# Kernel optimization log

Measured on AMD Instinct MI355X. Metric: run time of the kernel, lower is better.

Reference implementation:

```python
import jax, jax.numpy as jnp
import numpy as np

D_EMBED = 768
D_HEAD = 64
B, S = 4, 4096


def setup_inputs() -> dict:
    key = jax.random.key(0)
    ks = jax.random.split(key, 8)
    x = jax.random.normal(ks[0], (B, S, D_EMBED), dtype=jnp.float32)
    mask = jax.random.randint(ks[1], (B, S), 0, 2, dtype=jnp.int32)
    s = 1.0 / np.sqrt(D_EMBED)
    Wq = jax.random.normal(ks[2], (D_EMBED, D_HEAD), dtype=jnp.float32) * s
    bq = jnp.zeros((D_HEAD,), dtype=jnp.float32)
    Wk = jax.random.normal(ks[3], (D_EMBED, D_HEAD), dtype=jnp.float32) * s
    bk = jnp.zeros((D_HEAD,), dtype=jnp.float32)
    Wv = jax.random.normal(ks[4], (D_EMBED, D_HEAD), dtype=jnp.float32) * s
    bv = jnp.zeros((D_HEAD,), dtype=jnp.float32)
    return {"x": x, "mask": mask, "Wq": Wq, "bq": bq, "Wk": Wk, "bk": bk, "Wv": Wv, "bv": bv}


def reference(x, mask, Wq, bq, Wk, bk, Wv, bv):
    # x: [B,S,D_EMBED], mask: [B,S] (0 = masked)
    q = x @ Wq + bq          # [B,S,Dh]
    k = x @ Wk + bk
    v = x @ Wv + bv
    scale = jnp.float32(1.0 / np.sqrt(D_HEAD))
    scores = jnp.einsum('bsd,btd->bst', q, k) * scale   # [B,S,S]
    scores = jnp.where(mask[:, None, :] == 0, jnp.float32(-1e9), scores)
    probs = jax.nn.softmax(scores, axis=-1)
    return jnp.einsum('bst,btd->bsd', probs, v)          # [B,S,Dh]
```

## Files before the change

### kernel.cpp

```cpp
#include <hip/hip_runtime.h>
#include <hip/hip_bf16.h>
#include <stdint.h>

#define B_  4
#define S_  4096
#define DE  768
#define DH  64
#define NQKV 192
#define MFIX 8.0f
#define NSPLIT 8
#define QG 128

typedef __attribute__((ext_vector_type(8))) short    short8;
typedef __attribute__((ext_vector_type(4))) float    floatx4;
typedef __attribute__((ext_vector_type(4))) unsigned short ushort4v;

__device__ unsigned short g_wt[NQKV * DE];
__device__ unsigned short g_q [B_ * S_ * DH];
__device__ unsigned short g_k [B_ * S_ * DH];
__device__ unsigned short g_vt[B_ * DH * S_];
__device__ float g_po[(size_t)B_ * 32 * NSPLIT * QG * DH];
__device__ float g_pl[(size_t)B_ * 32 * NSPLIT * QG];

__device__ __forceinline__ unsigned short f2bf_h(float f) {
    union { float f; uint32_t u; } v; v.f = f;
    return (unsigned short)((v.u + 0x8000u) >> 16);
}

__global__ __launch_bounds__(256) void pack_w(
    const float* __restrict__ Wq, const float* __restrict__ Wk,
    const float* __restrict__ Wv)
{
    int idx = blockIdx.x * 256 + threadIdx.x;
    if (idx >= NQKV * DE) return;
    int n = idx / DE;
    int d = idx - n * DE;
    float w;
    if      (n < 64)  w = Wq[d * 64 + n];
    else if (n < 128) w = Wk[d * 64 + (n - 64)];
    else              w = Wv[d * 64 + (n - 128)];
    g_wt[idx] = f2bf_h(w);
}

__global__ __launch_bounds__(256, 3) void qkv_mfma(
    const float* __restrict__ x,
    const float* __restrict__ bq, const float* __restrict__ bk,
    const float* __restrict__ bv)
{
    __shared__ unsigned short xs[32][776];
    const int t    = threadIdx.x;
    const int lane = t & 63;
    const int wave = t >> 6;
    const int c16  = lane & 15;
    const int quad = lane >> 4;
    const int n0   = wave * 48;
    const int row0 = blockIdx.x * 32;

    {
        const int xr = t >> 3;
        const int xc = t & 7;
        const float* xrow = x + (size_t)(row0 + xr) * DE;
        #pragma unroll
        for (int j = 0; j < 24; ++j) {
            int c4 = xc + 8 * j;
            floatx4 v = *(const floatx4*)&xrow[c4 * 4];
            ushort4v h;
            #pragma unroll
            for (int k = 0; k < 4; ++k) h[k] = f2bf_h(v[k]);
            *(ushort4v*)&xs[xr][c4 * 4] = h;
        }
    }
    __syncthreads();

    floatx4 acc[6];
    #pragma unroll
    for (int i = 0; i < 6; ++i) acc[i] = (floatx4){0.f,0.f,0.f,0.f};

    short8 wb[6];
    #pragma unroll
    for (int nt = 0; nt < 3; ++nt) {
        const unsigned short* wrow = g_wt + (size_t)(n0 + nt * 16 + c16) * DE + quad * 8;
        wb[2 * nt]     = *(const short8*)wrow;
        wb[2 * nt + 1] = *(const short8*)(wrow + 32);
    }

    #pragma unroll
    for (int ks = 0; ks < 12; ++ks) {
        const int k0  = ks * 64;
        const int k0n = (ks < 11) ? k0 + 64 : 0;
        short8 nwb[6];
        #pragma unroll
        for (int nt = 0; nt < 3; ++nt) {
            const unsigned short* wrow = g_wt + (size_t)(n0 + nt * 16 + c16) * DE + k0n + quad * 8;
            nwb[2 * nt]     = *(const short8*)wrow;
            nwb[2 * nt + 1] = *(const short8*)(wrow + 32);
        }
        short8 a00 = *(const short8*)&xs[c16][k0 + quad * 8];
        short8 a01 = *(const short8*)&xs[c16][k0 + quad * 8 + 32];
        short8 a10 = *(const short8*)&xs[16 + c16][k0 + quad * 8];
        short8 a11 = *(const short8*)&xs[16 + c16][k0 + quad * 8 + 32];
        #pragma unroll
        for (int nt = 0; nt < 3; ++nt) {
            acc[nt]     = __builtin_amdgcn_mfma_f32_16x16x32_bf16(a00, wb[2 * nt],     acc[nt],     0, 0, 0);
            acc[nt]     = __builtin_amdgcn_mfma_f32_16x16x32_bf16(a01, wb[2 * nt + 1], acc[nt],     0, 0, 0);
            acc[3 + nt] = __builtin_amdgcn_mfma_f32_16x16x32_bf16(a10, wb[2 * nt],     acc[3 + nt], 0, 0, 0);
            acc[3 + nt] = __builtin_amdgcn_mfma_f32_16x16x32_bf16(a11, wb[2 * nt + 1], acc[3 + nt], 0, 0, 0);
        }
        #pragma unroll
        for (int j = 0; j < 6; ++j) wb[j] = nwb[j];
    }

    #pragma unroll
    for (int m = 0; m < 2; ++m) {
        const int tokb = row0 + m * 16 + quad * 4;
        #pragma unroll
        for (int nt = 0; nt < 3; ++nt) {
            int n = n0 + nt * 16 + c16;
            int which = n >> 6;
            int d = n & 63;
            float bias = (which == 0) ? bq[d] : (which == 1) ? bk[d] : bv[d];
            floatx4 a = acc[m * 3 + nt];
            if (which == 0) {
                #pragma unroll
                for (int r = 0; r < 4; ++r)
                    g_q[(size_t)(tokb + r) * DH + d] = f2bf_h((a[r] + bias) * 0.125f);
            } else if (which == 1) {
                #pragma unroll
                for (int r = 0; r < 4; ++r)
                    g_k[(size_t)(tokb + r) * DH + d] = f2bf_h(a[r] + bias);
            } else {
                ushort4v h;
                #pragma unroll
                for (int r = 0; r < 4; ++r) h[r] = f2bf_h(a[r] + bias);
                int b = tokb >> 12;
                int tloc = tokb & (S_ - 1);
                *(ushort4v*)&g_vt[((size_t)b * DH + d) * S_ + tloc] = h;
            }
        }
    }
}

__global__ __launch_bounds__(256, 4) void attn_kernel(const int* __restrict__ mask)
{
    __shared__ short8 ksv[512];
    __shared__ short8 vsv[512];
    __shared__ unsigned short sp[4 * 2 * 16 * 72];

    const int t    = threadIdx.x;
    const int lane = t & 63;
    const int wave = t >> 6;
    const int c16  = lane & 15;
    const int quad = lane >> 4;
    const int qg   = blockIdx.x;
    const int b    = blockIdx.y;
    const int s    = blockIdx.z;
    const size_t tok0 = (size_t)b * S_;
    const int pidx = (b * 32 + qg) * NSPLIT + s;

    const unsigned short* kbase = g_k + tok0 * DH;
    const unsigned short* vtb   = g_vt + (size_t)b * DH * S_;
    const int* mrow = mask + b * S_;

    short8 aq0A, aq1A, aq0B, aq1B;
    {
        const unsigned short* qrA = g_q + (tok0 + qg * QG + wave * 32 + c16) * DH;
        aq0A = *(const short8*)(qrA + quad * 8);
        aq1A = *(const short8*)(qrA + quad * 8 + 32);
        const unsigned short* qrB = qrA + 16 * DH;
        aq0B = *(const short8*)(qrB + quad * 8);
        aq1B = *(const short8*)(qrB + quad * 8 + 32);
    }

    short8 ones;
    #pragma unroll
    for (int j = 0; j < 8; ++j) ones[j] = (short)0x3F80;

    floatx4 acc[2][5];
    #pragma unroll
    for (int qt = 0; qt < 2; ++qt)
        #pragma unroll
        for (int i = 0; i < 5; ++i) acc[qt][i] = (floatx4){0.f,0.f,0.f,0.f};

    const int kbeg = s * (S_ / NSPLIT);
    const int kend = kbeg + S_ / NSPLIT;

    #define SPI(w, qt, row, col) ((((w) * 2 + (qt)) * 16 + (row)) * 72 + (col))

    const int sr  = t >> 2;
    const int sp0 = (t & 3) * 2;
    const int sw0 = sr * 8 + (sp0 ^ (sr & 7));
    const int sw1 = sr * 8 + ((sp0 + 1) ^ (sr & 7));

    short8 kpre0, kpre1, vpre0, vpre1;
    int mpre[4];
    {
        const unsigned short* kr = kbase + (size_t)(kbeg + sr) * DH + sp0 * 8;
        kpre0 = *(const short8*)kr;
        kpre1 = *(const short8*)(kr + 8);
        const unsigned short* vr = vtb + (size_t)sr * S_ + kbeg + sp0 * 8;
        vpre0 = *(const short8*)vr;
        vpre1 = *(const short8*)(vr + 8);
        #pragma unroll
        for (int nt = 0; nt < 4; ++nt) mpre[nt] = mrow[kbeg + c16 + 16 * nt];
    }

    for (int tb = kbeg; tb < kend; tb += 64) {
        __syncthreads();
        ksv[sw0] = kpre0;
        ksv[sw1] = kpre1;
        vsv[sw0] = vpre0;
        vsv[sw1] = vpre1;
        int mv[4];
        #pragma unroll
        for (int nt = 0; nt < 4; ++nt) mv[nt] = mpre[nt];
        __syncthreads();

        {
            const int tbn = (tb + 64 < kend) ? tb + 64 : kbeg;
            const unsigned short* kr = kbase + (size_t)(tbn + sr) * DH + sp0 * 8;
            kpre0 = *(const short8*)kr;
            kpre1 = *(const short8*)(kr + 8);
            const unsigned short* vr = vtb + (size_t)sr * S_ + tbn + sp0 * 8;
            vpre0 = *(const short8*)vr;
            vpre1 = *(const short8*)(vr + 8);
            #pragma unroll
            for (int nt = 0; nt < 4; ++nt) mpre[nt] = mrow[tbn + c16 + 16 * nt];
        }

        #pragma unroll
        for (int nt = 0; nt < 4; ++nt) {
            const int key = c16 + 16 * nt;
            short8 kb0 = ksv[key * 8 + (quad ^ (key & 7))];
            short8 kb1 = ksv[key * 8 + ((quad + 4) ^ (key & 7))];
            floatx4 zA = (floatx4){0.f,0.f,0.f,0.f};
            zA = __builtin_amdgcn_mfma_f32_16x16x32_bf16(aq0A, kb0, zA, 0, 0, 0);
            zA = __builtin_amdgcn_mfma_f32_16x16x32_bf16(aq1A, kb1, zA, 0, 0, 0);
            floatx4 zB = (floatx4){0.f,0.f,0.f,0.f};
            zB = __builtin_amdgcn_mfma_f32_16x16x32_bf16(aq0B, kb0, zB, 0, 0, 0);
            zB = __builtin_amdgcn_mfma_f32_16x16x32_bf16(aq1B, kb1, zB, 0, 0, 0);
            #pragma unroll
            for (int r = 0; r < 4; ++r) {
                float sA = mv[nt] ? zA[r] : -1e9f;
                float sB = mv[nt] ? zB[r] : -1e9f;
                sp[SPI(wave, 0, quad * 4 + r, key)] = f2bf_h(__expf(sA - MFIX));
                sp[SPI(wave, 1, quad * 4 + r, key)] = f2bf_h(__expf(sB - MFIX));
            }
        }

        #pragma unroll
        for (int h = 0; h < 2; ++h) {
            short8 apA = *(const short8*)&sp[SPI(wave, 0, c16, quad * 8 + 32 * h)];
            short8 apB = *(const short8*)&sp[SPI(wave, 1, c16, quad * 8 + 32 * h)];
            #pragma unroll
            for (int nt = 0; nt < 4; ++nt) {
                const int d = c16 + 16 * nt;
                short8 vb = vsv[d * 8 + ((h * 4 + quad) ^ (d & 7))];
                acc[0][nt] = __builtin_amdgcn_mfma_f32_16x16x32_bf16(apA, vb, acc[0][nt], 0, 0, 0);
                acc[1][nt] = __builtin_amdgcn_mfma_f32_16x16x32_bf16(apB, vb, acc[1][nt], 0, 0, 0);
            }
            acc[0][4] = __builtin_amdgcn_mfma_f32_16x16x32_bf16(apA, ones, acc[0][4], 0, 0, 0);
            acc[1][4] = __builtin_amdgcn_mfma_f32_16x16x32_bf16(apB, ones, acc[1][4], 0, 0, 0);
        }
    }

    float* po = g_po + (size_t)pidx * (QG * DH) + (wave * 32) * 64;
    #pragma unroll
    for (int qt = 0; qt < 2; ++qt)
        #pragma unroll
        for (int nt = 0; nt < 4; ++nt)
            #pragma unroll
            for (int r = 0; r < 4; ++r)
                po[(qt * 16 + quad * 4 + r) * 64 + c16 + 16 * nt] = acc[qt][nt][r];
    if (c16 == 0) {
        float* pl = g_pl + (size_t)pidx * QG + wave * 32;
        #pragma unroll
        for (int qt = 0; qt < 2; ++qt)
            #pragma unroll
            for (int r = 0; r < 4; ++r)
                pl[qt * 16 + quad * 4 + r] = acc[qt][4][r];
    }
}

__global__ __launch_bounds__(256) void combine(float* __restrict__ out)
{
    const int idx = blockIdx.x * 256 + threadIdx.x;
    const int d4  = idx & 15;
    const int tok = idx >> 4;
    const int qq  = tok & (QG - 1);
    const int qg  = (tok >> 7) & 31;
    const int b   = tok >> 12;
    const int base = (b * 32 + qg) * NSPLIT;
    floatx4 os = (floatx4){0.f,0.f,0.f,0.f};
    float ls = 0.f;
    #pragma unroll
    for (int s = 0; s < NSPLIT; ++s) {
        os += *(const floatx4*)&g_po[(size_t)(base + s) * (QG * DH) + qq * 64 + d4 * 4];
        ls += g_pl[(size_t)(base + s) * QG + qq];
    }
    float inv = 1.0f / ls;
    floatx4 r;
    #pragma unroll
    for (int j = 0; j < 4; ++j) r[j] = os[j] * inv;
    *(floatx4*)&out[(size_t)tok * DH + d4 * 4] = r;
}

extern "C" void kernel_launch(void* const* d_in, const int* in_sizes, int n_in,
                              void* d_out, int out_size, void* d_ws, size_t ws_size,
                              hipStream_t stream) {
    const float* x   = (const float*)d_in[0];
    const int*   msk = (const int*)  d_in[1];
    const float* Wq  = (const float*)d_in[2];
    const float* bq  = (const float*)d_in[3];
    const float* Wk  = (const float*)d_in[4];
    const float* bk  = (const float*)d_in[5];
    const float* Wv  = (const float*)d_in[6];
    const float* bv  = (const float*)d_in[7];
    float* out = (float*)d_out;

    pack_w<<<dim3((NQKV * DE + 255) / 256), 256, 0, stream>>>(Wq, Wk, Wv);
    qkv_mfma<<<dim3(B_ * S_ / 32), 256, 0, stream>>>(x, bq, bk, bv);
    attn_kernel<<<dim3(S_ / QG, B_, NSPLIT), 256, 0, stream>>>(msk);
    combine<<<dim3(B_ * S_ * DH / 1024), 256, 0, stream>>>(out);
}
```

Measured before the change: 151.2 us.

## Double query tile per block and store split partials in fp16

Each attention block now handles 256 queries (64 per wave, four 16-row MFMA tiles) instead of 128. Every K/V tile staged in shared memory is reused across twice as many queries, halving K/V global traffic and staging work. Partial outputs are written as fp16 rather than fp32, halving the scratch traffic between the attention and combine kernels. In exchange, register and LDS use per block grow (launch bounds drop to 2 blocks per CU), the grid has half as many blocks, and the fp16 partials lose some precision and could overflow for large unnormalized sums.

```diff
diff --git a/kernel.cpp b/kernel.cpp
--- a/kernel.cpp
+++ b/kernel.cpp
@@ -1,5 +1,6 @@
 #include <hip/hip_runtime.h>
 #include <hip/hip_bf16.h>
+#include <hip/hip_fp16.h>
 #include <stdint.h>
 
 #define B_  4
@@ -9,7 +10,7 @@
 #define NQKV 192
 #define MFIX 8.0f
 #define NSPLIT 8
-#define QG 128
+#define QG 256
 
 typedef __attribute__((ext_vector_type(8))) short    short8;
 typedef __attribute__((ext_vector_type(4))) float    floatx4;
@@ -19,8 +20,8 @@
 __device__ unsigned short g_q [B_ * S_ * DH];
 __device__ unsigned short g_k [B_ * S_ * DH];
 __device__ unsigned short g_vt[B_ * DH * S_];
-__device__ float g_po[(size_t)B_ * 32 * NSPLIT * QG * DH];
-__device__ float g_pl[(size_t)B_ * 32 * NSPLIT * QG];
+__device__ __half g_po[(size_t)B_ * (S_ / QG) * NSPLIT * QG * DH];
+__device__ float  g_pl[(size_t)B_ * (S_ / QG) * NSPLIT * QG];
 
 __device__ __forceinline__ unsigned short f2bf_h(float f) {
     union { float f; uint32_t u; } v; v.f = f;
@@ -140,11 +141,11 @@
     }
 }
 
-__global__ __launch_bounds__(256, 4) void attn_kernel(const int* __restrict__ mask)
+__global__ __launch_bounds__(256, 2) void attn_kernel(const int* __restrict__ mask)
 {
     __shared__ short8 ksv[512];
     __shared__ short8 vsv[512];
-    __shared__ unsigned short sp[4 * 2 * 16 * 72];
+    __shared__ unsigned short sp[4 * 4 * 16 * 72];
 
     const int t    = threadIdx.x;
     const int lane = t & 63;
@@ -155,36 +156,34 @@
     const int b    = blockIdx.y;
     const int s    = blockIdx.z;
     const size_t tok0 = (size_t)b * S_;
-    const int pidx = (b * 32 + qg) * NSPLIT + s;
+    const int pidx = (b * (S_ / QG) + qg) * NSPLIT + s;
 
     const unsigned short* kbase = g_k + tok0 * DH;
     const unsigned short* vtb   = g_vt + (size_t)b * DH * S_;
     const int* mrow = mask + b * S_;
 
-    short8 aq0A, aq1A, aq0B, aq1B;
-    {
-        const unsigned short* qrA = g_q + (tok0 + qg * QG + wave * 32 + c16) * DH;
-        aq0A = *(const short8*)(qrA + quad * 8);
-        aq1A = *(const short8*)(qrA + quad * 8 + 32);
-        const unsigned short* qrB = qrA + 16 * DH;
-        aq0B = *(const short8*)(qrB + quad * 8);
-        aq1B = *(const short8*)(qrB + quad * 8 + 32);
+    short8 aq[4][2];
+    #pragma unroll
+    for (int qt = 0; qt < 4; ++qt) {
+        const unsigned short* qr = g_q + (tok0 + qg * QG + wave * 64 + qt * 16 + c16) * DH;
+        aq[qt][0] = *(const short8*)(qr + quad * 8);
+        aq[qt][1] = *(const short8*)(qr + quad * 8 + 32);
     }
 
     short8 ones;
     #pragma unroll
     for (int j = 0; j < 8; ++j) ones[j] = (short)0x3F80;
 
-    floatx4 acc[2][5];
-    #pragma unroll
-    for (int qt = 0; qt < 2; ++qt)
+    floatx4 acc[4][5];
+    #pragma unroll
+    for (int qt = 0; qt < 4; ++qt)
         #pragma unroll
         for (int i = 0; i < 5; ++i) acc[qt][i] = (floatx4){0.f,0.f,0.f,0.f};
 
     const int kbeg = s * (S_ / NSPLIT);
     const int kend = kbeg + S_ / NSPLIT;
 
-    #define SPI(w, qt, row, col) ((((w) * 2 + (qt)) * 16 + (row)) * 72 + (col))
+    #define SPI(w, qt, row, col) ((((w) * 4 + (qt)) * 16 + (row)) * 72 + (col))
 
     const int sr  = t >> 2;
     const int sp0 = (t & 3) * 2;
@@ -232,52 +231,56 @@
             const int key = c16 + 16 * nt;
             short8 kb0 = ksv[key * 8 + (quad ^ (key & 7))];
             short8 kb1 = ksv[key * 8 + ((quad + 4) ^ (key & 7))];
-            floatx4 zA = (floatx4){0.f,0.f,0.f,0.f};
-            zA = __builtin_amdgcn_mfma_f32_16x16x32_bf16(aq0A, kb0, zA, 0, 0, 0);
-            zA = __builtin_amdgcn_mfma_f32_16x16x32_bf16(aq1A, kb1, zA, 0, 0, 0);
-            floatx4 zB = (floatx4){0.f,0.f,0.f,0.f};
-            zB = __builtin_amdgcn_mfma_f32_16x16x32_bf16(aq0B, kb0, zB, 0, 0, 0);
-            zB = __builtin_amdgcn_mfma_f32_16x16x32_bf16(aq1B, kb1, zB, 0, 0, 0);
-            #pragma unroll
-            for (int r = 0; r < 4; ++r) {
-                float sA = mv[nt] ? zA[r] : -1e9f;
-                float sB = mv[nt] ? zB[r] : -1e9f;
-                sp[SPI(wave, 0, quad * 4 + r, key)] = f2bf_h(__expf(sA - MFIX));
-                sp[SPI(wave, 1, quad * 4 + r, key)] = f2bf_h(__expf(sB - MFIX));
+            #pragma unroll
+            for (int qt = 0; qt < 4; ++qt) {
+                floatx4 z = (floatx4){0.f,0.f,0.f,0.f};
+                z = __builtin_amdgcn_mfma_f32_16x16x32_bf16(aq[qt][0], kb0, z, 0, 0, 0);
+                z = __builtin_amdgcn_mfma_f32_16x16x32_bf16(aq[qt][1], kb1, z, 0, 0, 0);
+                #pragma unroll
+                for (int r = 0; r < 4; ++r) {
+                    float sv = mv[nt] ? z[r] : -1e9f;
+                    sp[SPI(wave, qt, quad * 4 + r, key)] = f2bf_h(__expf(sv - MFIX));
+                }
             }
         }
 
         #pragma unroll
         for (int h = 0; h < 2; ++h) {
-            short8 apA = *(const short8*)&sp[SPI(wave, 0, c16, quad * 8 + 32 * h)];
-            short8 apB = *(const short8*)&sp[SPI(wave, 1, c16, quad * 8 + 32 * h)];
+            short8 ap[4];
+            #pragma unroll
+            for (int qt = 0; qt < 4; ++qt)
+                ap[qt] = *(const short8*)&sp[SPI(wave, qt, c16, quad * 8 + 32 * h)];
             #pragma unroll
             for (int nt = 0; nt < 4; ++nt) {
                 const int d = c16 + 16 * nt;
                 short8 vb = vsv[d * 8 + ((h * 4 + quad) ^ (d & 7))];
-                acc[0][nt] = __builtin_amdgcn_mfma_f32_16x16x32_bf16(apA, vb, acc[0][nt], 0, 0, 0);
-                acc[1][nt] = __builtin_amdgcn_mfma_f32_16x16x32_bf16(apB, vb, acc[1][nt], 0, 0, 0);
+                #pragma unroll
+                for (int qt = 0; qt < 4; ++qt)
+                    acc[qt][nt] = __builtin_amdgcn_mfma_f32_16x16x32_bf16(ap[qt], vb, acc[qt][nt], 0, 0, 0);
             }
-            acc[0][4] = __builtin_amdgcn_mfma_f32_16x16x32_bf16(apA, ones, acc[0][4], 0, 0, 0);
-            acc[1][4] = __builtin_amdgcn_mfma_f32_16x16x32_bf16(apB, ones, acc[1][4], 0, 0, 0);
-        }
-    }
-
-    float* po = g_po + (size_t)pidx * (QG * DH) + (wave * 32) * 64;
-    #pragma unroll
-    for (int qt = 0; qt < 2; ++qt)
+            #pragma unroll
+            for (int qt = 0; qt < 4; ++qt)
+                acc[qt][4] = __builtin_amdgcn_mfma_f32_16x16x32_bf16(ap[qt], ones, acc[qt][4], 0, 0, 0);
+        }
+    }
+
+    __half* po = g_po + (size_t)pidx * (QG * DH);
+    #pragma unroll
+    for (int qt = 0; qt < 4; ++qt) {
+        const int qrow = wave * 64 + qt * 16 + quad * 4;
         #pragma unroll
         for (int nt = 0; nt < 4; ++nt)
             #pragma unroll
             for (int r = 0; r < 4; ++r)
-                po[(qt * 16 + quad * 4 + r) * 64 + c16 + 16 * nt] = acc[qt][nt][r];
+                po[(qrow + r) * DH + c16 + 16 * nt] = __float2half(acc[qt][nt][r]);
+    }
     if (c16 == 0) {
-        float* pl = g_pl + (size_t)pidx * QG + wave * 32;
-        #pragma unroll
-        for (int qt = 0; qt < 2; ++qt)
+        float* pl = g_pl + (size_t)pidx * QG;
+        #pragma unroll
+        for (int qt = 0; qt < 4; ++qt)
             #pragma unroll
             for (int r = 0; r < 4; ++r)
-                pl[qt * 16 + quad * 4 + r] = acc[qt][4][r];
+                pl[wave * 64 + qt * 16 + quad * 4 + r] = acc[qt][4][r];
     }
 }
 
@@ -287,14 +290,16 @@
     const int d4  = idx & 15;
     const int tok = idx >> 4;
     const int qq  = tok & (QG - 1);
-    const int qg  = (tok >> 7) & 31;
+    const int qg  = (tok >> 8) & (S_ / QG - 1);
     const int b   = tok >> 12;
-    const int base = (b * 32 + qg) * NSPLIT;
+    const int base = (b * (S_ / QG) + qg) * NSPLIT;
     floatx4 os = (floatx4){0.f,0.f,0.f,0.f};
     float ls = 0.f;
     #pragma unroll
     for (int s = 0; s < NSPLIT; ++s) {
-        os += *(const floatx4*)&g_po[(size_t)(base + s) * (QG * DH) + qq * 64 + d4 * 4];
+        const __half* pp = g_po + (size_t)(base + s) * (QG * DH) + qq * 64 + d4 * 4;
+        #pragma unroll
+        for (int j = 0; j < 4; ++j) os[j] += __half2float(pp[j]);
         ls += g_pl[(size_t)(base + s) * QG + qq];
     }
     float inv = 1.0f / ls;
```

New measurement: 155.3 us. 2.7% more time.
